# Kernel optimization log

Measured on AMD Instinct MI355X. Metric: run time of the kernel, lower is better.

The kernel has to match this reference:

```python
import jax, jax.numpy as jnp
import numpy as np

B, N, S, F0, C, NOUT = 16, 64, 4, 8, 32, 1
N_VALID = 48  # valid (unpadded) nodes per graph


def setup_inputs() -> dict:
    key = jax.random.key(0)
    ks = jax.random.split(key, 12)
    valid = (jnp.arange(N) < N_VALID).astype(jnp.float32)  # [N]
    # node features, zero for padded nodes; last column is the binary mask
    x_feat = jax.random.normal(ks[0], (B, N, F0), dtype=jnp.float32) * valid[None, :, None]
    x = jnp.concatenate([x_feat, jnp.broadcast_to(valid[None, :, None], (B, N, 1))], axis=-1)
    # sparse-ish binary adjacency (avg degree ~ 0.1*N), zeroed on padded rows/cols
    a = (jax.random.uniform(ks[1], (B, N, N)) < 0.1).astype(jnp.float32)
    a = a * valid[None, :, None] * valid[None, None, :]
    # edge features, only on existing edges
    e = jax.random.normal(ks[2], (B, N, N, S), dtype=jnp.float32) * a[..., None]
    sc = 0.1
    return {
        "x": x, "a": a, "e": e,
        # ECCConv 1: F_in = F0 -> C
        "w1_kern": jax.random.normal(ks[3], (S, C * F0), dtype=jnp.float32) * sc,
        "b1_kern": jnp.zeros((C * F0,), jnp.float32),
        "w1_root": jax.random.normal(ks[4], (F0, C), dtype=jnp.float32) * sc,
        "b1": jnp.zeros((C,), jnp.float32),
        # ECCConv 2: F_in = C -> C
        "w2_kern": jax.random.normal(ks[5], (S, C * C), dtype=jnp.float32) * sc,
        "b2_kern": jnp.zeros((C * C,), jnp.float32),
        "w2_root": jax.random.normal(ks[6], (C, C), dtype=jnp.float32) * sc,
        "b2": jnp.zeros((C,), jnp.float32),
        # readout dense
        "w_dense": jax.random.normal(ks[7], (C, NOUT), dtype=jnp.float32) * sc,
        "b_dense": jnp.zeros((NOUT,), jnp.float32),
    }


def _ecc(x, a, e, wk, bk, wr, b, mask):
    # spektral ECCConv, batch mode
    Bb, Nn = x.shape[0], x.shape[1]
    Fin = x.shape[-1]
    Cc = wr.shape[1]
    # per-edge filter weights from edge features: [B,N,N,C,Fin]
    kernel = (e @ wk + bk).reshape(Bb, Nn, Nn, Cc, Fin)
    # output[b,t,c] = sum_{i,f} kernel[b,t,i,c,f] * a[b,t,i] * x[b,i,f]
    msg = jnp.einsum("btixy,bti,biy->btx", kernel, a, x)
    out = msg + x @ wr + b
    out = out * mask[..., None]  # keras mask applied before activation
    return jax.nn.relu(out)


def reference(x, a, e, w1_kern, b1_kern, w1_root, b1,
              w2_kern, b2_kern, w2_root, b2, w_dense, b_dense):
    # GraphMasking: strip last feature column, use it as node mask
    mask = x[..., -1]      # [B,N]
    h = x[..., :-1]        # [B,N,F0]
    h = _ecc(h, a, e, w1_kern, b1_kern, w1_root, b1, mask)
    h = _ecc(h, a, e, w2_kern, b2_kern, w2_root, b2, mask)
    pooled = jnp.sum(h * mask[..., None], axis=1)  # GlobalSumPool with mask -> [B,C]
    return pooled @ w_dense + b_dense              # [B, n_out]
```

## Files before the change

kernel.cpp:

```cpp
#include <hip/hip_runtime.h>
#include <hip/hip_bf16.h>

#define NT 1024

constexpr int B_ = 16, N_ = 64, S_ = 4, F0_ = 8, C_ = 32;
constexpr int MAXE = 32;

typedef __attribute__((ext_vector_type(8))) short short8;
typedef __attribute__((ext_vector_type(4))) float f32x4;

__device__ __forceinline__ unsigned short f2bf(float x) {
    __hip_bfloat16 h = __float2bfloat16(x);
    return *reinterpret_cast<unsigned short*>(&h);
}

template<int F, int SFP>
__device__ __forceinline__ void stage_w(int tid, const float* __restrict__ wk,
                                        const float* __restrict__ bk,
                                        const float* __restrict__ wr,
                                        unsigned short* wT) {
    constexpr int SF = 6 * F;
    for (int idx = tid; idx < C_ * SF; idx += NT) {
        int c = idx / SF, sf = idx - c * SF;
        int s = sf / F, f = sf - s * F;
        float v;
        if (s < 4)       v = wk[(s * C_ + c) * F + f];
        else if (s == 4) v = bk[c * F + f];
        else             v = wr[f * C_ + c];
        wT[c * SFP + sf] = f2bf(v);
    }
}

template<int F, int LOG2F, int SFP>
__device__ __forceinline__ void u_phase(int tid, const float* hin,
                                        const float4* ec4,
                                        const unsigned char* nbr_idx,
                                        const int* nbr_cnt,
                                        unsigned short* u_bf) {
    for (int pair = tid; pair < N_ * F; pair += NT) {
        int t = pair >> LOG2F;
        int f = pair & (F - 1);
        float u0 = 0.f, u1 = 0.f, u2 = 0.f, u3 = 0.f, u4 = 0.f;
        const int cnt = nbr_cnt[t];
        for (int j = 0; j < cnt; ++j) {
            int i = nbr_idx[t * MAXE + j];
            float hv = hin[i * F + f];
            float4 ev = ec4[t * MAXE + j];
            u0 = fmaf(ev.x, hv, u0);
            u1 = fmaf(ev.y, hv, u1);
            u2 = fmaf(ev.z, hv, u2);
            u3 = fmaf(ev.w, hv, u3);
            u4 += hv;
        }
        unsigned short* ut = u_bf + t * SFP;
        ut[0 * F + f] = f2bf(u0);
        ut[1 * F + f] = f2bf(u1);
        ut[2 * F + f] = f2bf(u2);
        ut[3 * F + f] = f2bf(u3);
        ut[4 * F + f] = f2bf(u4);
        ut[5 * F + f] = f2bf(hin[t * F + f]);
    }
}

template<int SFP, int KSTEPS>
__device__ __forceinline__ f32x4 mfma_tile(int lane, int mt, int nt,
                                           const unsigned short* u_bf,
                                           const unsigned short* wT) {
    const int quad = lane >> 4, l16 = lane & 15;
    f32x4 acc = {0.f, 0.f, 0.f, 0.f};
    const unsigned short* arow = u_bf + (mt * 16 + l16) * SFP;
    const unsigned short* brow = wT + (nt * 16 + l16) * SFP;
#pragma unroll
    for (int kk = 0; kk < KSTEPS; ++kk) {
        const int kb = kk * 32 + quad * 8;
        short8 av = *reinterpret_cast<const short8*>(arow + kb);
        short8 bv = *reinterpret_cast<const short8*>(brow + kb);
        acc = __builtin_amdgcn_mfma_f32_16x16x32_bf16(av, bv, acc, 0, 0, 0);
    }
    return acc;
}

__global__ __launch_bounds__(NT) void ecc_fused(
    const float* __restrict__ x,  const float* __restrict__ a,  const float* __restrict__ e,
    const float* __restrict__ w1k, const float* __restrict__ b1k,
    const float* __restrict__ w1r, const float* __restrict__ b1v,
    const float* __restrict__ w2k, const float* __restrict__ b2k,
    const float* __restrict__ w2r, const float* __restrict__ b2v,
    const float* __restrict__ wd,  const float* __restrict__ bd,
    float* __restrict__ out)
{
    __shared__ float x_sh[N_ * F0_];
    __shared__ float mask_sh[N_];
    __shared__ float h_sh[N_ * C_];
    __shared__ __align__(16) unsigned short u1_bf[N_ * 72];
    __shared__ __align__(16) unsigned short u2_bf[N_ * 200];
    __shared__ __align__(16) unsigned short wT1[C_ * 72];
    __shared__ __align__(16) unsigned short wT2[C_ * 200];
    __shared__ __align__(16) float4 ec4[N_ * MAXE];
    __shared__ unsigned char nbr_idx[N_ * MAXE];
    __shared__ int nbr_cnt[N_];
    __shared__ float b1_sh[C_], b2_sh[C_], wd_sh[C_];
    __shared__ float red_sh[8];

    const int b   = blockIdx.x;
    const int tid = threadIdx.x;
    const float* eb  = e + (size_t)b * N_ * N_ * S_;
    const float* a_g = a + (size_t)b * N_ * N_;

    {
        const int wv = tid >> 6, lane = tid & 63;
        float  av[4];
        float4 ev[4];
#pragma unroll
        for (int r = 0; r < 4; ++r) {
            const int t = wv * 4 + r;
            av[r] = a_g[t * N_ + lane];
            ev[r] = *reinterpret_cast<const float4*>(eb + (size_t)(t * N_ + lane) * S_);
        }
#pragma unroll
        for (int r = 0; r < 4; ++r) {
            const int t = wv * 4 + r;
            const unsigned long long m = __ballot(av[r] != 0.f);
            if (lane == 0) {
                int cnt = (int)__popcll(m);
                nbr_cnt[t] = cnt > MAXE ? MAXE : cnt;
            }
            if (av[r] != 0.f) {
                int pos = (int)__popcll(m & ((1ull << lane) - 1ull));
                if (pos < MAXE) {
                    nbr_idx[t * MAXE + pos] = (unsigned char)lane;
                    ec4[t * MAXE + pos] = ev[r];
                }
            }
        }
    }
    for (int idx = tid; idx < N_ * (F0_ + 1); idx += NT) {
        int t = idx / 9, j = idx - t * 9;
        float v = x[(b * N_ + t) * 9 + j];
        if (j == F0_) mask_sh[t] = v;
        else          x_sh[t * F0_ + j] = v;
    }
    stage_w<8, 72>(tid, w1k, b1k, w1r, wT1);
    stage_w<32, 200>(tid, w2k, b2k, w2r, wT2);
    if (tid < C_) { b1_sh[tid] = b1v[tid]; b2_sh[tid] = b2v[tid]; wd_sh[tid] = wd[tid]; }
    for (int idx = tid; idx < (N_ + C_) * 16; idx += NT) {
        int row = idx >> 4, k = idx & 15;
        if (row < N_) u1_bf[row * 72 + 48 + k] = 0;
        else          wT1[(row - N_) * 72 + 48 + k] = 0;
    }
    __syncthreads();

    u_phase<8, 3, 72>(tid, x_sh, ec4, nbr_idx, nbr_cnt, u1_bf);
    __syncthreads();

    {
        const int wv = tid >> 6;
        if (wv < 8) {
            const int lane = tid & 63, quad = lane >> 4, l16 = lane & 15;
            const int mt = wv >> 1, nt = wv & 1;
            f32x4 acc = mfma_tile<72, 2>(lane, mt, nt, u1_bf, wT1);
            const int cc = nt * 16 + l16;
            const float bc = b1_sh[cc];
#pragma unroll
            for (int r = 0; r < 4; ++r) {
                const int tt = mt * 16 + quad * 4 + r;
                float v = (acc[r] + bc) * mask_sh[tt];
                h_sh[tt * C_ + cc] = v > 0.f ? v : 0.f;
            }
        }
    }
    __syncthreads();

    u_phase<32, 5, 200>(tid, h_sh, ec4, nbr_idx, nbr_cnt, u2_bf);
    __syncthreads();

    {
        const int wv = tid >> 6;
        float partial = 0.f;
        if (wv < 8) {
            const int lane = tid & 63, quad = lane >> 4, l16 = lane & 15;
            const int mt = wv >> 1, nt = wv & 1;
            f32x4 acc = mfma_tile<200, 6>(lane, mt, nt, u2_bf, wT2);
            const int cc = nt * 16 + l16;
            const float bc = b2_sh[cc];
            const float wc = wd_sh[cc];
#pragma unroll
            for (int r = 0; r < 4; ++r) {
                const int tt = mt * 16 + quad * 4 + r;
                float v = (acc[r] + bc) * mask_sh[tt];
                partial += (v > 0.f ? v : 0.f) * wc;
            }
#pragma unroll
            for (int off = 32; off > 0; off >>= 1)
                partial += __shfl_down(partial, off, 64);
            if (lane == 0) red_sh[wv] = partial;
        }
    }
    __syncthreads();
    if (tid == 0) {
        float s = bd[0];
#pragma unroll
        for (int w = 0; w < 8; ++w) s += red_sh[w];
        out[b] = s;
    }
}

extern "C" void kernel_launch(void* const* d_in, const int* in_sizes, int n_in,
                              void* d_out, int out_size, void* d_ws, size_t ws_size,
                              hipStream_t stream) {
    ecc_fused<<<B_, NT, 0, stream>>>(
        (const float*)d_in[0],  (const float*)d_in[1],  (const float*)d_in[2],
        (const float*)d_in[3],  (const float*)d_in[4],  (const float*)d_in[5],
        (const float*)d_in[6],  (const float*)d_in[7],  (const float*)d_in[8],
        (const float*)d_in[9],  (const float*)d_in[10], (const float*)d_in[11],
        (const float*)d_in[12], (float*)d_out);
}
```

Measured before the change: 87.12 us.

## Reassociate ECC as dense edge-matrix MFMA after projecting node features by weights

Drops the sparse neighbor-list gather. Each layer now first projects node features by the stacked per-edge-feature, bias and root weights with MFMA (X·W). It then multiplies dense bf16 edge-feature and adjacency matrices by those projections with a second MFMA. This removes the scalar serial neighbor loop and its irregular shared-memory gathers, at the cost of dense work over all 64x64 entries and extra bf16 rounding of the intermediate projections.

```diff
diff --git a/kernel.cpp b/kernel.cpp
--- a/kernel.cpp
+++ b/kernel.cpp
@@ -4,7 +4,12 @@
 #define NT 1024
 
 constexpr int B_ = 16, N_ = 64, S_ = 4, F0_ = 8, C_ = 32;
-constexpr int MAXE = 32;
+
+constexpr int ESTR = 72;
+constexpr int EMAT = N_ * ESTR;
+constexpr int XSTR = 40;
+constexpr int WSTR = 40;
+constexpr int PSTR = 72;
 
 typedef __attribute__((ext_vector_type(8))) short short8;
 typedef __attribute__((ext_vector_type(4))) float f32x4;
@@ -13,69 +18,49 @@
     __hip_bfloat16 h = __float2bfloat16(x);
     return *reinterpret_cast<unsigned short*>(&h);
 }
-
-template<int F, int SFP>
-__device__ __forceinline__ void stage_w(int tid, const float* __restrict__ wk,
-                                        const float* __restrict__ bk,
-                                        const float* __restrict__ wr,
-                                        unsigned short* wT) {
-    constexpr int SF = 6 * F;
-    for (int idx = tid; idx < C_ * SF; idx += NT) {
-        int c = idx / SF, sf = idx - c * SF;
-        int s = sf / F, f = sf - s * F;
-        float v;
-        if (s < 4)       v = wk[(s * C_ + c) * F + f];
-        else if (s == 4) v = bk[c * F + f];
-        else             v = wr[f * C_ + c];
-        wT[c * SFP + sf] = f2bf(v);
-    }
-}
-
-template<int F, int LOG2F, int SFP>
-__device__ __forceinline__ void u_phase(int tid, const float* hin,
-                                        const float4* ec4,
-                                        const unsigned char* nbr_idx,
-                                        const int* nbr_cnt,
-                                        unsigned short* u_bf) {
-    for (int pair = tid; pair < N_ * F; pair += NT) {
-        int t = pair >> LOG2F;
-        int f = pair & (F - 1);
-        float u0 = 0.f, u1 = 0.f, u2 = 0.f, u3 = 0.f, u4 = 0.f;
-        const int cnt = nbr_cnt[t];
-        for (int j = 0; j < cnt; ++j) {
-            int i = nbr_idx[t * MAXE + j];
-            float hv = hin[i * F + f];
-            float4 ev = ec4[t * MAXE + j];
-            u0 = fmaf(ev.x, hv, u0);
-            u1 = fmaf(ev.y, hv, u1);
-            u2 = fmaf(ev.z, hv, u2);
-            u3 = fmaf(ev.w, hv, u3);
-            u4 += hv;
-        }
-        unsigned short* ut = u_bf + t * SFP;
-        ut[0 * F + f] = f2bf(u0);
-        ut[1 * F + f] = f2bf(u1);
-        ut[2 * F + f] = f2bf(u2);
-        ut[3 * F + f] = f2bf(u3);
-        ut[4 * F + f] = f2bf(u4);
-        ut[5 * F + f] = f2bf(hin[t * F + f]);
-    }
-}
-
-template<int SFP, int KSTEPS>
-__device__ __forceinline__ f32x4 mfma_tile(int lane, int mt, int nt,
-                                           const unsigned short* u_bf,
-                                           const unsigned short* wT) {
-    const int quad = lane >> 4, l16 = lane & 15;
+__device__ __forceinline__ float bf2f(unsigned short u) {
+    unsigned int v = ((unsigned int)u) << 16;
+    float f;
+    __builtin_memcpy(&f, &v, 4);
+    return f;
+}
+
+__device__ __forceinline__ void stepA(int wv, int lane,
+                                      const unsigned short* XHm,
+                                      const unsigned short* WT,
+                                      unsigned short* Pb) {
+    const int l16 = lane & 15, quad = lane >> 4;
+    const int mt = wv & 3, nt0 = (wv >> 2) * 3;
+    short8 av = *reinterpret_cast<const short8*>(XHm + (mt * 16 + l16) * XSTR + quad * 8);
+#pragma unroll
+    for (int q = 0; q < 3; ++q) {
+        const int nt = nt0 + q;
+        short8 bv = *reinterpret_cast<const short8*>(WT + (nt * 16 + l16) * WSTR + quad * 8);
+        f32x4 acc = {0.f, 0.f, 0.f, 0.f};
+        acc = __builtin_amdgcn_mfma_f32_16x16x32_bf16(av, bv, acc, 0, 0, 0);
+        ushort4 pk;
+        pk.x = f2bf(acc[0]); pk.y = f2bf(acc[1]);
+        pk.z = f2bf(acc[2]); pk.w = f2bf(acc[3]);
+        *reinterpret_cast<ushort4*>(Pb + (nt * 16 + l16) * PSTR + mt * 16 + quad * 4) = pk;
+    }
+}
+
+__device__ __forceinline__ f32x4 stepB_mm(int wv, int lane,
+                                          const unsigned short* EA,
+                                          const unsigned short* Pb) {
+    const int l16 = lane & 15, quad = lane >> 4;
+    const int mt = wv >> 1, nt = wv & 1;
     f32x4 acc = {0.f, 0.f, 0.f, 0.f};
-    const unsigned short* arow = u_bf + (mt * 16 + l16) * SFP;
-    const unsigned short* brow = wT + (nt * 16 + l16) * SFP;
-#pragma unroll
-    for (int kk = 0; kk < KSTEPS; ++kk) {
-        const int kb = kk * 32 + quad * 8;
-        short8 av = *reinterpret_cast<const short8*>(arow + kb);
-        short8 bv = *reinterpret_cast<const short8*>(brow + kb);
-        acc = __builtin_amdgcn_mfma_f32_16x16x32_bf16(av, bv, acc, 0, 0, 0);
+#pragma unroll
+    for (int s = 0; s < 5; ++s) {
+        const unsigned short* ar = EA + s * EMAT + (mt * 16 + l16) * ESTR;
+        const unsigned short* br = Pb + (s * 32 + nt * 16 + l16) * PSTR;
+#pragma unroll
+        for (int kk = 0; kk < 2; ++kk) {
+            short8 av = *reinterpret_cast<const short8*>(ar + kk * 32 + quad * 8);
+            short8 bv = *reinterpret_cast<const short8*>(br + kk * 32 + quad * 8);
+            acc = __builtin_amdgcn_mfma_f32_16x16x32_bf16(av, bv, acc, 0, 0, 0);
+        }
     }
     return acc;
 }
@@ -89,105 +74,105 @@
     const float* __restrict__ wd,  const float* __restrict__ bd,
     float* __restrict__ out)
 {
-    __shared__ float x_sh[N_ * F0_];
+    __shared__ __align__(16) unsigned short EA[5 * EMAT];
+    __shared__ __align__(16) unsigned short XH[N_ * XSTR];
+    __shared__ __align__(16) unsigned short W1T[192 * WSTR];
+    __shared__ __align__(16) unsigned short W2T[192 * WSTR];
+    __shared__ __align__(16) unsigned short Pb[192 * PSTR];
     __shared__ float mask_sh[N_];
-    __shared__ float h_sh[N_ * C_];
-    __shared__ __align__(16) unsigned short u1_bf[N_ * 72];
-    __shared__ __align__(16) unsigned short u2_bf[N_ * 200];
-    __shared__ __align__(16) unsigned short wT1[C_ * 72];
-    __shared__ __align__(16) unsigned short wT2[C_ * 200];
-    __shared__ __align__(16) float4 ec4[N_ * MAXE];
-    __shared__ unsigned char nbr_idx[N_ * MAXE];
-    __shared__ int nbr_cnt[N_];
     __shared__ float b1_sh[C_], b2_sh[C_], wd_sh[C_];
     __shared__ float red_sh[8];
 
     const int b   = blockIdx.x;
     const int tid = threadIdx.x;
-    const float* eb  = e + (size_t)b * N_ * N_ * S_;
-    const float* a_g = a + (size_t)b * N_ * N_;
+    const int wv  = tid >> 6, lane = tid & 63;
+    const float* eb = e + (size_t)b * N_ * N_ * S_;
+    const float* ag = a + (size_t)b * N_ * N_;
 
     {
-        const int wv = tid >> 6, lane = tid & 63;
+        float4 ev[4];
         float  av[4];
-        float4 ev[4];
 #pragma unroll
         for (int r = 0; r < 4; ++r) {
             const int t = wv * 4 + r;
-            av[r] = a_g[t * N_ + lane];
             ev[r] = *reinterpret_cast<const float4*>(eb + (size_t)(t * N_ + lane) * S_);
+            av[r] = ag[t * N_ + lane];
         }
 #pragma unroll
         for (int r = 0; r < 4; ++r) {
             const int t = wv * 4 + r;
-            const unsigned long long m = __ballot(av[r] != 0.f);
-            if (lane == 0) {
-                int cnt = (int)__popcll(m);
-                nbr_cnt[t] = cnt > MAXE ? MAXE : cnt;
-            }
-            if (av[r] != 0.f) {
-                int pos = (int)__popcll(m & ((1ull << lane) - 1ull));
-                if (pos < MAXE) {
-                    nbr_idx[t * MAXE + pos] = (unsigned char)lane;
-                    ec4[t * MAXE + pos] = ev[r];
-                }
-            }
-        }
-    }
-    for (int idx = tid; idx < N_ * (F0_ + 1); idx += NT) {
-        int t = idx / 9, j = idx - t * 9;
-        float v = x[(b * N_ + t) * 9 + j];
+            EA[0 * EMAT + t * ESTR + lane] = f2bf(ev[r].x);
+            EA[1 * EMAT + t * ESTR + lane] = f2bf(ev[r].y);
+            EA[2 * EMAT + t * ESTR + lane] = f2bf(ev[r].z);
+            EA[3 * EMAT + t * ESTR + lane] = f2bf(ev[r].w);
+            EA[4 * EMAT + t * ESTR + lane] = f2bf(av[r]);
+        }
+    }
+    if (tid < N_ * 9) {
+        const int t = tid / 9, j = tid - t * 9;
+        const float v = x[(b * N_ + t) * 9 + j];
         if (j == F0_) mask_sh[t] = v;
-        else          x_sh[t * F0_ + j] = v;
-    }
-    stage_w<8, 72>(tid, w1k, b1k, w1r, wT1);
-    stage_w<32, 200>(tid, w2k, b2k, w2r, wT2);
+        else          XH[t * XSTR + j] = f2bf(v);
+    }
+    for (int idx = tid; idx < N_ * 24; idx += NT) {
+        const int t = idx / 24, k = idx - t * 24;
+        XH[t * XSTR + 8 + k] = 0;
+    }
+    for (int idx = tid; idx < 192 * 32; idx += NT) {
+        const int n = idx >> 5, k = idx & 31;
+        const int s = n >> 5,  c = n & 31;
+        float v1, v2;
+        if (k >= F0_)    v1 = 0.f;
+        else if (s < 4)  v1 = w1k[s * (C_ * F0_) + c * F0_ + k];
+        else if (s == 4) v1 = b1k[c * F0_ + k];
+        else             v1 = w1r[k * C_ + c];
+        if (s < 4)       v2 = w2k[s * (C_ * C_) + c * C_ + k];
+        else if (s == 4) v2 = b2k[c * C_ + k];
+        else             v2 = w2r[k * C_ + c];
+        W1T[n * WSTR + k] = f2bf(v1);
+        W2T[n * WSTR + k] = f2bf(v2);
+    }
     if (tid < C_) { b1_sh[tid] = b1v[tid]; b2_sh[tid] = b2v[tid]; wd_sh[tid] = wd[tid]; }
-    for (int idx = tid; idx < (N_ + C_) * 16; idx += NT) {
-        int row = idx >> 4, k = idx & 15;
-        if (row < N_) u1_bf[row * 72 + 48 + k] = 0;
-        else          wT1[(row - N_) * 72 + 48 + k] = 0;
-    }
-    __syncthreads();
-
-    u_phase<8, 3, 72>(tid, x_sh, ec4, nbr_idx, nbr_cnt, u1_bf);
+    __syncthreads();
+
+    stepA(wv, lane, XH, W1T, Pb);
+    __syncthreads();
+
+    if (wv < 8) {
+        const int l16 = lane & 15, quad = lane >> 4;
+        const int mt = wv >> 1, nt = wv & 1;
+        f32x4 acc = stepB_mm(wv, lane, EA, Pb);
+        const int c = nt * 16 + l16;
+        ushort4 p5 = *reinterpret_cast<const ushort4*>(Pb + (160 + c) * PSTR + mt * 16 + quad * 4);
+        const unsigned short p5a[4] = {p5.x, p5.y, p5.z, p5.w};
+        const float bc = b1_sh[c];
+#pragma unroll
+        for (int r = 0; r < 4; ++r) {
+            const int t = mt * 16 + quad * 4 + r;
+            float v = (acc[r] + bc + bf2f(p5a[r])) * mask_sh[t];
+            XH[t * XSTR + c] = f2bf(v > 0.f ? v : 0.f);
+        }
+    }
+    __syncthreads();
+
+    stepA(wv, lane, XH, W2T, Pb);
     __syncthreads();
 
     {
-        const int wv = tid >> 6;
-        if (wv < 8) {
-            const int lane = tid & 63, quad = lane >> 4, l16 = lane & 15;
-            const int mt = wv >> 1, nt = wv & 1;
-            f32x4 acc = mfma_tile<72, 2>(lane, mt, nt, u1_bf, wT1);
-            const int cc = nt * 16 + l16;
-            const float bc = b1_sh[cc];
-#pragma unroll
-            for (int r = 0; r < 4; ++r) {
-                const int tt = mt * 16 + quad * 4 + r;
-                float v = (acc[r] + bc) * mask_sh[tt];
-                h_sh[tt * C_ + cc] = v > 0.f ? v : 0.f;
-            }
-        }
-    }
-    __syncthreads();
-
-    u_phase<32, 5, 200>(tid, h_sh, ec4, nbr_idx, nbr_cnt, u2_bf);
-    __syncthreads();
-
-    {
-        const int wv = tid >> 6;
         float partial = 0.f;
         if (wv < 8) {
-            const int lane = tid & 63, quad = lane >> 4, l16 = lane & 15;
+            const int l16 = lane & 15, quad = lane >> 4;
             const int mt = wv >> 1, nt = wv & 1;
-            f32x4 acc = mfma_tile<200, 6>(lane, mt, nt, u2_bf, wT2);
-            const int cc = nt * 16 + l16;
-            const float bc = b2_sh[cc];
-            const float wc = wd_sh[cc];
+            f32x4 acc = stepB_mm(wv, lane, EA, Pb);
+            const int c = nt * 16 + l16;
+            ushort4 p5 = *reinterpret_cast<const ushort4*>(Pb + (160 + c) * PSTR + mt * 16 + quad * 4);
+            const unsigned short p5a[4] = {p5.x, p5.y, p5.z, p5.w};
+            const float bc = b2_sh[c];
+            const float wc = wd_sh[c];
 #pragma unroll
             for (int r = 0; r < 4; ++r) {
-                const int tt = mt * 16 + quad * 4 + r;
-                float v = (acc[r] + bc) * mask_sh[tt];
+                const int t = mt * 16 + quad * 4 + r;
+                float v = (acc[r] + bc + bf2f(p5a[r])) * mask_sh[t];
                 partial += (v > 0.f ? v : 0.f) * wc;
             }
 #pragma unroll
```

Result: faster. 85.18 us (-2.2%).
